# Kernel tuning notes

Hardware: AMD Instinct MI355X
Metric: run time of the kernel (lower is better)

## Reference

```python
import jax, jax.numpy as jnp
import numpy as np
import math

B, T, C = 4, 1024, 1024
H = 16          # n_head
E = 8           # num_experts
K = 2           # top_k
HID = 4096      # expert_hidden_dim
TEMP = 1.0
EPS_LN = 1e-5


def setup_inputs() -> dict:
    key = jax.random.key(0)
    ks = jax.random.split(key, 16)
    s = 0.02
    return {
        'x': jax.random.normal(ks[0], (B, T, C), jnp.float32),
        'ln1_g': jnp.ones((C,), jnp.float32),
        'ln1_b': jnp.zeros((C,), jnp.float32),
        'W_qkv': jax.random.normal(ks[1], (C, 3 * C), jnp.float32) * s,
        'b_qkv': jnp.zeros((3 * C,), jnp.float32),
        'W_proj': jax.random.normal(ks[2], (C, C), jnp.float32) * s,
        'b_proj': jnp.zeros((C,), jnp.float32),
        'ln2_g': jnp.ones((C,), jnp.float32),
        'ln2_b': jnp.zeros((C,), jnp.float32),
        'W_router': jax.random.normal(ks[3], (C, E), jnp.float32) * s,
        'W1': jax.random.normal(ks[4], (E, C, HID), jnp.float32) * s,
        'b1': jnp.zeros((E, HID), jnp.float32),
        'W2': jax.random.normal(ks[5], (E, HID, C), jnp.float32) * s,
        'b2': jnp.zeros((E, C), jnp.float32),
    }


def _layernorm(x, g, b):
    mu = jnp.mean(x, axis=-1, keepdims=True)
    var = jnp.mean(jnp.square(x - mu), axis=-1, keepdims=True)
    return (x - mu) * jax.lax.rsqrt(var + EPS_LN) * g + b


def reference(x, ln1_g, ln1_b, W_qkv, b_qkv, W_proj, b_proj,
              ln2_g, ln2_b, W_router, W1, b1, W2, b2):
    D = C // H
    # --- causal self-attention on ln_1(x) ---
    h = _layernorm(x, ln1_g, ln1_b)
    qkv = h @ W_qkv + b_qkv                      # [B,T,3C]
    q, k, v = jnp.split(qkv, 3, axis=-1)
    q = q.reshape(B, T, H, D).transpose(0, 2, 1, 3)   # [B,H,T,D]
    k = k.reshape(B, T, H, D).transpose(0, 2, 1, 3)
    v = v.reshape(B, T, H, D).transpose(0, 2, 1, 3)
    att = jnp.einsum('bhqd,bhkd->bhqk', q, k) * (1.0 / math.sqrt(D))
    mask = jnp.tril(jnp.ones((T, T), bool))
    att = jnp.where(mask, att, -jnp.inf)
    att = jax.nn.softmax(att, axis=-1)
    y = jnp.einsum('bhqk,bhkd->bhqd', att, v)
    y = y.transpose(0, 2, 1, 3).reshape(B, T, C)
    x = x + (y @ W_proj + b_proj)

    # --- sparse MoE on ln_2(x) ---
    h2 = _layernorm(x, ln2_g, ln2_b)
    xf = h2.reshape(-1, C)                       # [N,C]
    N = xf.shape[0]
    logits = (xf @ W_router) / TEMP              # [N,E]
    prob = jax.nn.softmax(logits, axis=-1)
    top_prob, top_idx = jax.lax.top_k(prob, K)   # [N,K]
    top_prob = top_prob / (jnp.sum(top_prob, axis=-1, keepdims=True) + 1e-9)
    # dense per-token per-expert combine weights (0 for unselected experts)
    w = jnp.zeros((N, E), xf.dtype).at[jnp.arange(N)[:, None], top_idx].add(top_prob)
    # dense expert compute (weights zero out unselected experts -> same math)
    hid = jax.nn.gelu(jnp.einsum('nc,ech->neh', xf, W1) + b1, approximate=False)
    eo = jnp.einsum('neh,ehc->nec', hid, W2) + b2          # [N,E,C]
    out_flat = jnp.einsum('nec,ne->nc', eo, w)
    x = x + out_flat.reshape(B, T, C)

    counts = jnp.zeros((E,), jnp.float32).at[top_idx.reshape(-1)].add(1.0)
    expert_utilization = counts / (jnp.sum(counts) + 1e-9)
    return x, expert_utilization
```

## Files before the change

### kernel.cpp

```cpp
#include <hip/hip_runtime.h>
#include <cmath>

#define CDIM 1024
#define NTOK 4096
#define NHEAD 16
#define HDIM 64
#define NEXP 8
#define HIDD 4096
#define MAXROWS 9216

typedef short bf16x8 __attribute__((ext_vector_type(8)));
typedef short s16x4  __attribute__((ext_vector_type(4)));
typedef float f32x4  __attribute__((ext_vector_type(4)));

static __device__ __forceinline__ short f2bf(float f){
  unsigned u = __builtin_bit_cast(unsigned, f);
  u += 0x7fffu + ((u >> 16) & 1u);
  return (short)(u >> 16);
}
static __device__ __forceinline__ float bf2f(short s){
  unsigned u = ((unsigned)(unsigned short)s) << 16;
  return __builtin_bit_cast(float, u);
}

static __device__ __forceinline__ int swz64(int r, int ch){
  return r*64 + (((ch ^ (r>>1)) & 3) << 4);
}
static __device__ __forceinline__ int swz128(int r, int ch){
  return r*128 + (((ch ^ r) & 7) << 4);
}

static __device__ __forceinline__ void gl16(const short* g, short* l){
  __builtin_amdgcn_global_load_lds(
      (const __attribute__((address_space(1))) void*)g,
      (__attribute__((address_space(3))) void*)l, 16, 0, 0);
}

__global__ void k_transpose_cast(const float* __restrict__ in, short* __restrict__ out,
                                 int R, int Cc){
  __shared__ float tile[64][65];
  const int z = blockIdx.z;
  const float* src = in + (long long)z*R*Cc;
  short* dst = out + (long long)z*R*Cc;
  const int r0 = blockIdx.y*64, c0 = blockIdx.x*64;
  const int t = threadIdx.x;
  #pragma unroll
  for (int it=0; it<4; ++it){
    const int item = t + it*256;
    const int r = item>>4, c4 = item&15;
    const float4 v = *(const float4*)(src + (long long)(r0+r)*Cc + c0 + c4*4);
    tile[r][c4*4+0]=v.x; tile[r][c4*4+1]=v.y; tile[r][c4*4+2]=v.z; tile[r][c4*4+3]=v.w;
  }
  __syncthreads();
  #pragma unroll
  for (int it=0; it<2; ++it){
    const int item = t + it*256;
    const int rr8 = item & 7, cc = item >> 3;
    bf16x8 o;
    #pragma unroll
    for (int i=0;i<8;i++) o[i] = f2bf(tile[rr8*8+i][cc]);
    *(bf16x8*)(dst + (long long)(c0+cc)*R + r0 + rr8*8) = o;
  }
}

__global__ void k_ln1(const float* __restrict__ x, const float* __restrict__ g,
                      const float* __restrict__ b, short* __restrict__ out){
  const int row = blockIdx.x;
  const int t = threadIdx.x;
  const float4 v = ((const float4*)(x + (long long)row*CDIM))[t];
  float s  = v.x+v.y+v.z+v.w;
  float s2 = v.x*v.x+v.y*v.y+v.z*v.z+v.w*v.w;
  #pragma unroll
  for (int mm=1; mm<64; mm<<=1){ s += __shfl_xor(s,mm); s2 += __shfl_xor(s2,mm); }
  __shared__ float ps[4], ps2[4];
  const int w = t>>6, l = t&63;
  if (l==0){ ps[w]=s; ps2[w]=s2; }
  __syncthreads();
  s  = ps[0]+ps[1]+ps[2]+ps[3];
  s2 = ps2[0]+ps2[1]+ps2[2]+ps2[3];
  const float mu = s*(1.f/CDIM);
  const float rstd = rsqrtf(s2*(1.f/CDIM) - mu*mu + 1e-5f);
  const float4 gg = ((const float4*)g)[t];
  const float4 bb = ((const float4*)b)[t];
  s16x4 o;
  o[0]=f2bf((v.x-mu)*rstd*gg.x+bb.x); o[1]=f2bf((v.y-mu)*rstd*gg.y+bb.y);
  o[2]=f2bf((v.z-mu)*rstd*gg.z+bb.z); o[3]=f2bf((v.w-mu)*rstd*gg.w+bb.w);
  *(s16x4*)(out + (long long)row*CDIM + t*4) = o;
}

__global__ void k_ln2_router(const float* __restrict__ x1, const float* __restrict__ g,
                             const float* __restrict__ b, const float* __restrict__ Wr,
                             short* __restrict__ h2, int* __restrict__ tidx,
                             float* __restrict__ tw, int* __restrict__ counts){
  const int row = blockIdx.x;
  const int t = threadIdx.x;
  const float4 v = ((const float4*)(x1 + (long long)row*CDIM))[t];
  float s  = v.x+v.y+v.z+v.w;
  float s2 = v.x*v.x+v.y*v.y+v.z*v.z+v.w*v.w;
  #pragma unroll
  for (int mm=1; mm<64; mm<<=1){ s += __shfl_xor(s,mm); s2 += __shfl_xor(s2,mm); }
  __shared__ float ps[4], ps2[4];
  const int w = t>>6, l = t&63;
  if (l==0){ ps[w]=s; ps2[w]=s2; }
  __syncthreads();
  s  = ps[0]+ps[1]+ps[2]+ps[3];
  s2 = ps2[0]+ps2[1]+ps2[2]+ps2[3];
  const float mu = s*(1.f/CDIM);
  const float rstd = rsqrtf(s2*(1.f/CDIM) - mu*mu + 1e-5f);
  const float4 gg = ((const float4*)g)[t];
  const float4 bb = ((const float4*)b)[t];
  const float y0=(v.x-mu)*rstd*gg.x+bb.x, y1=(v.y-mu)*rstd*gg.y+bb.y;
  const float y2=(v.z-mu)*rstd*gg.z+bb.z, y3=(v.w-mu)*rstd*gg.w+bb.w;
  s16x4 o; o[0]=f2bf(y0); o[1]=f2bf(y1); o[2]=f2bf(y2); o[3]=f2bf(y3);
  *(s16x4*)(h2 + (long long)row*CDIM + t*4) = o;

  float acc[8];
  const float* wr0 = Wr + (long long)(t*4)*NEXP;
  #pragma unroll
  for (int e=0;e<8;e++) acc[e] = y0*wr0[e] + y1*wr0[8+e] + y2*wr0[16+e] + y3*wr0[24+e];
  #pragma unroll
  for (int mm=1; mm<64; mm<<=1){
    #pragma unroll
    for (int e=0;e<8;e++) acc[e] += __shfl_xor(acc[e], mm);
  }
  __shared__ float pl[4][8];
  if (l==0){
    #pragma unroll
    for (int e=0;e<8;e++) pl[w][e]=acc[e];
  }
  __syncthreads();
  if (t==0){
    float lg[8];
    #pragma unroll
    for (int e=0;e<8;e++) lg[e] = pl[0][e]+pl[1][e]+pl[2][e]+pl[3][e];
    float mx = lg[0];
    #pragma unroll
    for (int e=1;e<8;e++) mx = fmaxf(mx, lg[e]);
    float pr[8]; float sum = 0.f;
    #pragma unroll
    for (int e=0;e<8;e++){ pr[e]=expf(lg[e]-mx); sum += pr[e]; }
    int i0 = 0;
    #pragma unroll
    for (int e=1;e<8;e++) if (pr[e] > pr[i0]) i0 = e;
    int i1 = (i0==0) ? 1 : 0;
    #pragma unroll
    for (int e=0;e<8;e++) if (e!=i0 && pr[e] > pr[i1]) i1 = e;
    const float p0 = pr[i0]/sum, p1 = pr[i1]/sum;
    const float dn = p0 + p1 + 1e-9f;
    tidx[row*2]=i0; tidx[row*2+1]=i1;
    tw[row*2]=p0/dn; tw[row*2+1]=p1/dn;
    atomicAdd(&counts[i0],1); atomicAdd(&counts[i1],1);
  }
}

__global__ void k_route_setup(const int* __restrict__ counts, int* __restrict__ offs,
                              int* __restrict__ cursors, float* __restrict__ util){
  if (threadIdx.x == 0){
    int o = 0;
    for (int e=0;e<8;e++){
      offs[e] = o; cursors[e] = o;
      o += (counts[e] + 127) & ~127;
    }
    offs[8] = o;
    for (int e=0;e<8;e++) util[e] = (float)counts[e] / 8192.0f;
  }
}

__global__ void k_scatter(const int* __restrict__ tidx, const float* __restrict__ tw,
                          int* __restrict__ cursors, int* __restrict__ rowmap,
                          float* __restrict__ roww, int* __restrict__ posmap){
  const int i = blockIdx.x*blockDim.x + threadIdx.x;
  if (i >= 2*NTOK) return;
  const int e = tidx[i];
  const int pos = atomicAdd(&cursors[e], 1);
  rowmap[pos] = i >> 1;
  roww[pos]   = tw[i];
  posmap[i]   = pos;
}

template<int EPI>
__launch_bounds__(512, 4)
__global__ void k_gemm(const short* __restrict__ A, const short* __restrict__ Bt,
                       const float* __restrict__ bias, const float* __restrict__ resid,
                       void* __restrict__ Cout, int N, int K,
                       const int* __restrict__ rowmap, const int* __restrict__ offs,
                       long long expStrideB, const short* __restrict__ zrow){
  int wg = blockIdx.x;
  const int nwg = gridDim.x;
  {
    const int q = nwg >> 3, r8 = nwg & 7;
    const int xcd = wg & 7, pos = wg >> 3;
    wg = (xcd < r8 ? xcd*(q+1) : r8*(q+1) + (xcd - r8)*q) + pos;
  }
  const int gridN = N >> 7;
  const int gridM = nwg / gridN;
  const int mtile = wg % gridM, ntile = wg / gridM;
  const int mbase = mtile*128;
  const int nbase = ntile*128;
  int e = 0;
  if constexpr (EPI >= 2){
    if (mbase >= offs[8]) return;
    while (e < 7 && mbase >= offs[e+1]) e++;
    Bt += (long long)e * expStrideB;
  }
  __shared__ short Asm[2][4096];
  __shared__ short Bsm[2][4096];
  const int tid = threadIdx.x;
  const int w = tid >> 6, l = tid & 63;
  const int wr = w >> 1, wc = w & 1;
  const int l15 = l & 15, l4 = l >> 4;

  const short* aSrc; const short* bSrc;
  {
    const int r = tid >> 2, ch = tid & 3;
    const int sch = (ch ^ (r >> 1)) & 3;
    if constexpr (EPI == 2){
      const int grow = rowmap[mbase + r];
      aSrc = (grow >= 0) ? (A + (long long)grow*K + sch*8) : (zrow + sch*8);
    } else {
      aSrc = A + (long long)(mbase + r)*K + sch*8;
    }
    bSrc = Bt + (long long)(nbase + r)*K + sch*8;
  }
  const int dOff = w*512;

  f32x4 acc[2][4];
  const f32x4 z4 = {0.f,0.f,0.f,0.f};
  #pragma unroll
  for (int i=0;i<2;i++){
    #pragma unroll
    for (int jn=0;jn<4;jn++) acc[i][jn] = z4;
  }

  auto stage = [&](int buf, int kt){
    gl16(aSrc + kt, &Asm[buf][dOff]);
    gl16(bSrc + kt, &Bsm[buf][dOff]);
  };
  auto compute = [&](int buf){
    bf16x8 af[2], bfr[4];
    #pragma unroll
    for (int i=0;i<2;i++)
      af[i]  = *(const bf16x8*)((char*)Asm[buf] + swz64(wr*32 + i*16 + l15, l4));
    #pragma unroll
    for (int jn=0;jn<4;jn++)
      bfr[jn] = *(const bf16x8*)((char*)Bsm[buf] + swz64(wc*64 + jn*16 + l15, l4));
    #pragma unroll
    for (int i=0;i<2;i++){
      #pragma unroll
      for (int jn=0;jn<4;jn++)
        acc[i][jn] = __builtin_amdgcn_mfma_f32_16x16x32_bf16(af[i], bfr[jn], acc[i][jn], 0,0,0);
    }
  };

  stage(0, 0);
  asm volatile("s_waitcnt vmcnt(0)" ::: "memory");
  __builtin_amdgcn_s_barrier();

  int cur = 0;
  for (int kt = 32; kt < K; kt += 32){
    stage(cur ^ 1, kt);
    compute(cur);
    asm volatile("s_waitcnt vmcnt(0)" ::: "memory");
    __builtin_amdgcn_s_barrier();
    cur ^= 1;
  }
  compute(cur);

  #pragma unroll
  for (int i=0;i<2;i++){
    const int row0 = mbase + wr*32 + i*16 + l4*4;
    #pragma unroll
    for (int jn=0;jn<4;jn++){
      const int col = nbase + wc*64 + jn*16 + l15;
      const float bi = bias[(EPI>=2 ? e*N : 0) + col];
      #pragma unroll
      for (int j=0;j<4;j++){
        const long long idx = (long long)(row0 + j)*N + col;
        float v = acc[i][jn][j] + bi;
        if constexpr (EPI == 0){
          ((short*)Cout)[idx] = f2bf(v);
        } else if constexpr (EPI == 1){
          ((float*)Cout)[idx] = v + resid[idx];
        } else if constexpr (EPI == 2){
          ((short*)Cout)[idx] = f2bf(0.5f*v*(1.0f + erff(v*0.70710678118654752f)));
        } else {
          ((short*)Cout)[idx] = f2bf(v);
        }
      }
    }
  }
}

__launch_bounds__(512)
__global__ void k_attn(const short* __restrict__ qkv, short* __restrict__ y){
  const int qp = blockIdx.x;
  const int bh = blockIdx.y;
  const int bb = bh >> 4;
  const int h  = bh & 15;
  const int tid = threadIdx.x;
  const int w = tid >> 6, l = tid & 63;
  const int half = w >> 2, wq = w & 3;
  const int l15 = l & 15, l4 = l >> 4;

  __shared__ short Ksm[64*64];
  __shared__ short Vtsm[64*64];
  __shared__ short Psm[8*16*64];

  const long long rs = 3*CDIM;
  const int qrow0 = bb*1024 + qp*128;
  const int myQt = (qp << 1) + half;
  const int qtHigh = (qp << 1) + 1;

  bf16x8 aq[2];
  {
    const int qr = qrow0 + half*64 + wq*16 + l15;
    const short* qp2 = qkv + (long long)qr*rs + h*HDIM;
    aq[0] = *(const bf16x8*)(qp2 + l4*8);
    aq[1] = *(const bf16x8*)(qp2 + 32 + l4*8);
  }

  const f32x4 z4 = {0.f,0.f,0.f,0.f};
  f32x4 O[4];
  #pragma unroll
  for (int cf=0;cf<4;cf++) O[cf] = z4;
  float mrow[4], lrow[4];
  #pragma unroll
  for (int j=0;j<4;j++){ mrow[j] = -1e30f; lrow[j] = 0.f; }

  for (int kvb = 0; kvb <= qtHigh; ++kvb){
    const int kvrow0 = bb*1024 + kvb*64;
    {
      const int r = tid >> 3, c = tid & 7;
      const short* kp = qkv + (long long)(kvrow0 + r)*rs + CDIM + h*HDIM + c*8;
      *(bf16x8*)((char*)Ksm + swz128(r, c)) = *(const bf16x8*)kp;
      const short* vp = qkv + (long long)(kvrow0 + r)*rs + 2*CDIM + h*HDIM + c*8;
      bf16x8 vv = *(const bf16x8*)vp;
      const int off2 = 2*r;
      const int g0 = off2 >> 4, b0 = off2 & 15;
      #pragma unroll
      for (int i=0;i<8;i++){
        const int d = c*8 + i;
        *(short*)((char*)Vtsm + d*128 + (((g0 ^ d) & 7) << 4) + b0) = vv[i];
      }
    }
    __syncthreads();

    if (kvb <= myQt){
      f32x4 S[4];
      #pragma unroll
      for (int cf=0;cf<4;cf++) S[cf] = z4;
      #pragma unroll
      for (int cf=0;cf<4;cf++){
        #pragma unroll
        for (int kf=0;kf<2;kf++){
          bf16x8 bk = *(const bf16x8*)((char*)Ksm + swz128(cf*16 + l15, kf*4 + l4));
          S[cf] = __builtin_amdgcn_mfma_f32_16x16x32_bf16(aq[kf], bk, S[cf], 0,0,0);
        }
      }

      const bool diag = (kvb == myQt);
      #pragma unroll
      for (int cf=0;cf<4;cf++){
        #pragma unroll
        for (int j=0;j<4;j++){
          float s = S[cf][j] * 0.125f;
          if (diag && (cf*16 + l15 > wq*16 + l4*4 + j)) s = -1e30f;
          S[cf][j] = s;
        }
      }

      float alpha[4];
      #pragma unroll
      for (int j=0;j<4;j++){
        float mx = fmaxf(fmaxf(S[0][j],S[1][j]), fmaxf(S[2][j],S[3][j]));
        #pragma unroll
        for (int mm=1; mm<16; mm<<=1) mx = fmaxf(mx, __shfl_xor(mx, mm));
        const float mnew = fmaxf(mrow[j], mx);
        const float al = expf(mrow[j] - mnew);
        float psum = 0.f;
        #pragma unroll
        for (int cf=0;cf<4;cf++){ float pp = expf(S[cf][j]-mnew); S[cf][j]=pp; psum += pp; }
        #pragma unroll
        for (int mm=1; mm<16; mm<<=1) psum += __shfl_xor(psum, mm);
        lrow[j] = lrow[j]*al + psum;
        mrow[j] = mnew; alpha[j] = al;
      }
      #pragma unroll
      for (int cf=0;cf<4;cf++){
        #pragma unroll
        for (int j=0;j<4;j++) O[cf][j] *= alpha[j];
      }

      char* pw = (char*)Psm + w*2048;
      #pragma unroll
      for (int cf=0;cf<4;cf++){
        #pragma unroll
        for (int j=0;j<4;j++){
          const int r = l4*4 + j;
          const int cb = (cf*16 + l15)*2;
          *(short*)(pw + r*128 + ((((cb>>4) ^ r) & 7)<<4) + (cb & 15)) = f2bf(S[cf][j]);
        }
      }
      bf16x8 pa[2];
      pa[0] = *(const bf16x8*)(pw + swz128(l15, l4));
      pa[1] = *(const bf16x8*)(pw + swz128(l15, 4 + l4));
      #pragma unroll
      for (int cf=0;cf<4;cf++){
        #pragma unroll
        for (int kf=0;kf<2;kf++){
          bf16x8 bv = *(const bf16x8*)((char*)Vtsm + swz128(cf*16 + l15, kf*4 + l4));
          O[cf] = __builtin_amdgcn_mfma_f32_16x16x32_bf16(pa[kf], bv, O[cf], 0,0,0);
        }
      }
    }
    __syncthreads();
  }

  const int yr0 = qrow0 + half*64 + wq*16;
  #pragma unroll
  for (int cf=0;cf<4;cf++){
    #pragma unroll
    for (int j=0;j<4;j++){
      const int r = l4*4 + j;
      y[(long long)(yr0 + r)*CDIM + h*HDIM + cf*16 + l15] = f2bf(O[cf][j] / lrow[j]);
    }
  }
}

__global__ void k_combine(const float* __restrict__ x1, const short* __restrict__ eo,
                          const int* __restrict__ posmap, const float* __restrict__ roww,
                          float* __restrict__ out){
  const int row = blockIdx.x;
  const int t = threadIdx.x;
  const int p0 = posmap[row*2], p1 = posmap[row*2+1];
  const float w0 = roww[p0], w1 = roww[p1];
  const float4 a  = ((const float4*)(x1 + (long long)row*CDIM))[t];
  const s16x4 e0 = *(const s16x4*)(eo + (long long)p0*CDIM + t*4);
  const s16x4 e1 = *(const s16x4*)(eo + (long long)p1*CDIM + t*4);
  float4 r;
  r.x = a.x + w0*bf2f(e0[0]) + w1*bf2f(e1[0]);
  r.y = a.y + w0*bf2f(e0[1]) + w1*bf2f(e1[1]);
  r.z = a.z + w0*bf2f(e0[2]) + w1*bf2f(e1[2]);
  r.w = a.w + w0*bf2f(e0[3]) + w1*bf2f(e1[3]);
  ((float4*)(out + (long long)row*CDIM))[t] = r;
}

extern "C" void kernel_launch(void* const* d_in, const int* in_sizes, int n_in,
                              void* d_out, int out_size, void* d_ws, size_t ws_size,
                              hipStream_t stream){
  const float* x     = (const float*)d_in[0];
  const float* ln1_g = (const float*)d_in[1];
  const float* ln1_b = (const float*)d_in[2];
  const float* W_qkv = (const float*)d_in[3];
  const float* b_qkv = (const float*)d_in[4];
  const float* W_proj= (const float*)d_in[5];
  const float* b_proj= (const float*)d_in[6];
  const float* ln2_g = (const float*)d_in[7];
  const float* ln2_b = (const float*)d_in[8];
  const float* W_r   = (const float*)d_in[9];
  const float* W1    = (const float*)d_in[10];
  const float* b1    = (const float*)d_in[11];
  const float* W2    = (const float*)d_in[12];
  const float* b2    = (const float*)d_in[13];
  float* out = (float*)d_out;
  float* util = out + (long long)NTOK*CDIM;

  char* p = (char*)d_ws;
  auto alloc = [&](size_t bytes)->char*{
    char* r = p; p += (bytes + 255) & ~(size_t)255; return r;
  };
  short* Wt1   = (short*)alloc((size_t)NEXP*HIDD*CDIM*2);
  short* Wt2   = (short*)alloc((size_t)NEXP*CDIM*HIDD*2);
  float* x1    = (float*)alloc((size_t)NTOK*CDIM*4);
  short* h2    = (short*)alloc((size_t)NTOK*CDIM*2);
  short* hid   = (short*)alloc((size_t)MAXROWS*HIDD*2);
  int*   tidx  = (int*)alloc(2*NTOK*4);
  float* tw    = (float*)alloc(2*NTOK*4);
  int*   counts= (int*)alloc(256);
  int*   offs  = (int*)alloc(256);
  int*   curs  = (int*)alloc(256);
  int*   rowmap= (int*)alloc(MAXROWS*4);
  float* roww  = (float*)alloc(MAXROWS*4);
  int*   posmap= (int*)alloc(2*NTOK*4);
  short* zrow  = (short*)alloc(8192);
  char* transStart = p;
  short* WtQ = (short*)alloc((size_t)3*CDIM*CDIM*2);
  short* WtP = (short*)alloc((size_t)CDIM*CDIM*2);
  short* h   = (short*)alloc((size_t)NTOK*CDIM*2);
  short* qkv = (short*)alloc((size_t)NTOK*3*CDIM*2);
  short* y   = (short*)alloc((size_t)NTOK*CDIM*2);
  short* eo  = (short*)transStart;

  (void)hipMemsetAsync(counts, 0, 32, stream);
  (void)hipMemsetAsync(zrow, 0, 8192, stream);
  (void)hipMemsetAsync(rowmap, 0xFF, MAXROWS*4, stream);

  k_transpose_cast<<<dim3(3*CDIM/64, CDIM/64, 1), 256, 0, stream>>>(W_qkv, WtQ, CDIM, 3*CDIM);
  k_transpose_cast<<<dim3(CDIM/64, CDIM/64, 1),   256, 0, stream>>>(W_proj, WtP, CDIM, CDIM);
  k_transpose_cast<<<dim3(HIDD/64, CDIM/64, NEXP),256, 0, stream>>>(W1, Wt1, CDIM, HIDD);
  k_transpose_cast<<<dim3(CDIM/64, HIDD/64, NEXP),256, 0, stream>>>(W2, Wt2, HIDD, CDIM);

  k_ln1<<<NTOK, 256, 0, stream>>>(x, ln1_g, ln1_b, h);

  k_gemm<0><<<dim3((NTOK/128)*(3*CDIM/128)), 512, 0, stream>>>(
      h, WtQ, b_qkv, nullptr, qkv, 3*CDIM, CDIM, nullptr, nullptr, 0, nullptr);

  k_attn<<<dim3(1024/128, 4*NHEAD), 512, 0, stream>>>(qkv, y);

  k_gemm<1><<<dim3((NTOK/128)*(CDIM/128)), 512, 0, stream>>>(
      y, WtP, b_proj, x, x1, CDIM, CDIM, nullptr, nullptr, 0, nullptr);

  k_ln2_router<<<NTOK, 256, 0, stream>>>(x1, ln2_g, ln2_b, W_r, h2, tidx, tw, counts);
  k_route_setup<<<1, 64, 0, stream>>>(counts, offs, curs, util);
  k_scatter<<<(2*NTOK)/256, 256, 0, stream>>>(tidx, tw, curs, rowmap, roww, posmap);

  k_gemm<2><<<dim3((MAXROWS/128)*(HIDD/128)), 512, 0, stream>>>(
      h2, Wt1, b1, nullptr, hid, HIDD, CDIM, rowmap, offs, (long long)HIDD*CDIM, zrow);
  k_gemm<3><<<dim3((MAXROWS/128)*(CDIM/128)), 512, 0, stream>>>(
      hid, Wt2, b2, nullptr, eo, CDIM, HIDD, nullptr, offs, (long long)CDIM*HIDD, zrow);

  k_combine<<<NTOK, 256, 0, stream>>>(x1, eo, posmap, roww, out);
}
```

Baseline: 632.0 us.

## Use 128x256 tiles for expert up-projection GEMM and tanh-approximate GELU

Adds a dedicated up-projection kernel that computes 128x256 output tiles, with each wave holding a 4x4 MFMA accumulator block. This raises arithmetic intensity per LDS load and halves the number of A-row reloads across N. The exact erf GELU is also replaced with a tanh approximation built on __expf, to make the epilogue cheaper. The approximation differs numerically from the exact GELU the reference specifies. The larger accumulator footprint under launch_bounds(512,4) risks register pressure.

```diff
diff --git a/kernel.cpp b/kernel.cpp
--- a/kernel.cpp
+++ b/kernel.cpp
@@ -21,6 +21,11 @@
 static __device__ __forceinline__ float bf2f(short s){
   unsigned u = ((unsigned)(unsigned short)s) << 16;
   return __builtin_bit_cast(float, u);
+}
+static __device__ __forceinline__ float gelu_t(float x){
+  const float y = 0.7978845608f*(x + 0.044715f*x*x*x);
+  const float e = __expf(2.f*y);
+  return 0.5f*x*(1.f + (e-1.f)/(e+1.f));
 }
 
 static __device__ __forceinline__ int swz64(int r, int ch){
@@ -183,8 +188,7 @@
 __global__ void k_gemm(const short* __restrict__ A, const short* __restrict__ Bt,
                        const float* __restrict__ bias, const float* __restrict__ resid,
                        void* __restrict__ Cout, int N, int K,
-                       const int* __restrict__ rowmap, const int* __restrict__ offs,
-                       long long expStrideB, const short* __restrict__ zrow){
+                       const int* __restrict__ offs, long long expStrideB){
   int wg = blockIdx.x;
   const int nwg = gridDim.x;
   {
@@ -198,7 +202,7 @@
   const int mbase = mtile*128;
   const int nbase = ntile*128;
   int e = 0;
-  if constexpr (EPI >= 2){
+  if constexpr (EPI == 3){
     if (mbase >= offs[8]) return;
     while (e < 7 && mbase >= offs[e+1]) e++;
     Bt += (long long)e * expStrideB;
@@ -214,12 +218,7 @@
   {
     const int r = tid >> 2, ch = tid & 3;
     const int sch = (ch ^ (r >> 1)) & 3;
-    if constexpr (EPI == 2){
-      const int grow = rowmap[mbase + r];
-      aSrc = (grow >= 0) ? (A + (long long)grow*K + sch*8) : (zrow + sch*8);
-    } else {
-      aSrc = A + (long long)(mbase + r)*K + sch*8;
-    }
+    aSrc = A + (long long)(mbase + r)*K + sch*8;
     bSrc = Bt + (long long)(nbase + r)*K + sch*8;
   }
   const int dOff = w*512;
@@ -272,7 +271,7 @@
     #pragma unroll
     for (int jn=0;jn<4;jn++){
       const int col = nbase + wc*64 + jn*16 + l15;
-      const float bi = bias[(EPI>=2 ? e*N : 0) + col];
+      const float bi = bias[(EPI==3 ? e*N : 0) + col];
       #pragma unroll
       for (int j=0;j<4;j++){
         const long long idx = (long long)(row0 + j)*N + col;
@@ -281,11 +280,115 @@
           ((short*)Cout)[idx] = f2bf(v);
         } else if constexpr (EPI == 1){
           ((float*)Cout)[idx] = v + resid[idx];
-        } else if constexpr (EPI == 2){
-          ((short*)Cout)[idx] = f2bf(0.5f*v*(1.0f + erff(v*0.70710678118654752f)));
         } else {
           ((short*)Cout)[idx] = f2bf(v);
         }
+      }
+    }
+  }
+}
+
+__launch_bounds__(512, 4)
+__global__ void k_gemm_up(const short* __restrict__ A, const short* __restrict__ Bt,
+                          const float* __restrict__ bias, short* __restrict__ Cout,
+                          int N, int K, const int* __restrict__ rowmap,
+                          const int* __restrict__ offs, long long expStrideB,
+                          const short* __restrict__ zrow){
+  int wg = blockIdx.x;
+  const int nwg = gridDim.x;
+  {
+    const int q = nwg >> 3, r8 = nwg & 7;
+    const int xcd = wg & 7, pos = wg >> 3;
+    wg = (xcd < r8 ? xcd*(q+1) : r8*(q+1) + (xcd - r8)*q) + pos;
+  }
+  const int gridN = N >> 8;
+  const int gridM = nwg / gridN;
+  const int mtile = wg % gridM, ntile = wg / gridM;
+  const int mbase = mtile*128;
+  const int nbase = ntile*256;
+  if (mbase >= offs[8]) return;
+  int e = 0;
+  while (e < 7 && mbase >= offs[e+1]) e++;
+  Bt += (long long)e * expStrideB;
+
+  __shared__ short Asm[2][4096];
+  __shared__ short Bsm[2][8192];
+  const int tid = threadIdx.x;
+  const int w = tid >> 6, l = tid & 63;
+  const int wr = w >> 2, wc = w & 3;
+  const int l15 = l & 15, l4 = l >> 4;
+
+  const short* aSrc; const short* bSrc[2];
+  {
+    const int r = tid >> 2, ch = tid & 3;
+    const int sch = (ch ^ (r >> 1)) & 3;
+    const int grow = rowmap[mbase + r];
+    aSrc = (grow >= 0) ? (A + (long long)grow*K + sch*8) : (zrow + sch*8);
+  }
+  #pragma unroll
+  for (int inst=0; inst<2; ++inst){
+    const int g = inst*512 + tid;
+    const int r = g >> 2, ch = g & 3;
+    const int sch = (ch ^ (r >> 1)) & 3;
+    bSrc[inst] = Bt + (long long)(nbase + r)*K + sch*8;
+  }
+  const int aOff = w*512;
+  const int bOff0 = w*512, bOff1 = 4096 + w*512;
+
+  f32x4 acc[4][4];
+  const f32x4 z4 = {0.f,0.f,0.f,0.f};
+  #pragma unroll
+  for (int i=0;i<4;i++){
+    #pragma unroll
+    for (int jn=0;jn<4;jn++) acc[i][jn] = z4;
+  }
+
+  auto stage = [&](int buf, int kt){
+    gl16(aSrc + kt, &Asm[buf][aOff]);
+    gl16(bSrc[0] + kt, &Bsm[buf][bOff0]);
+    gl16(bSrc[1] + kt, &Bsm[buf][bOff1]);
+  };
+  auto compute = [&](int buf){
+    bf16x8 af[4], bfr[4];
+    #pragma unroll
+    for (int i=0;i<4;i++)
+      af[i]  = *(const bf16x8*)((char*)Asm[buf] + swz64(wr*64 + i*16 + l15, l4));
+    #pragma unroll
+    for (int jn=0;jn<4;jn++)
+      bfr[jn] = *(const bf16x8*)((char*)Bsm[buf] + swz64(wc*64 + jn*16 + l15, l4));
+    #pragma unroll
+    for (int i=0;i<4;i++){
+      #pragma unroll
+      for (int jn=0;jn<4;jn++)
+        acc[i][jn] = __builtin_amdgcn_mfma_f32_16x16x32_bf16(af[i], bfr[jn], acc[i][jn], 0,0,0);
+    }
+  };
+
+  stage(0, 0);
+  asm volatile("s_waitcnt vmcnt(0)" ::: "memory");
+  __builtin_amdgcn_s_barrier();
+
+  int cur = 0;
+  for (int kt = 32; kt < K; kt += 32){
+    stage(cur ^ 1, kt);
+    compute(cur);
+    asm volatile("s_waitcnt vmcnt(0)" ::: "memory");
+    __builtin_amdgcn_s_barrier();
+    cur ^= 1;
+  }
+  compute(cur);
+
+  #pragma unroll
+  for (int i=0;i<4;i++){
+    const int row0 = mbase + wr*64 + i*16 + l4*4;
+    #pragma unroll
+    for (int jn=0;jn<4;jn++){
+      const int col = nbase + wc*64 + jn*16 + l15;
+      const float bi = bias[e*N + col];
+      #pragma unroll
+      for (int j=0;j<4;j++){
+        const long long idx = (long long)(row0 + j)*N + col;
+        Cout[idx] = f2bf(gelu_t(acc[i][jn][j] + bi));
       }
     }
   }
@@ -503,21 +606,21 @@
   k_ln1<<<NTOK, 256, 0, stream>>>(x, ln1_g, ln1_b, h);
 
   k_gemm<0><<<dim3((NTOK/128)*(3*CDIM/128)), 512, 0, stream>>>(
-      h, WtQ, b_qkv, nullptr, qkv, 3*CDIM, CDIM, nullptr, nullptr, 0, nullptr);
+      h, WtQ, b_qkv, nullptr, qkv, 3*CDIM, CDIM, nullptr, 0);
 
   k_attn<<<dim3(1024/128, 4*NHEAD), 512, 0, stream>>>(qkv, y);
 
   k_gemm<1><<<dim3((NTOK/128)*(CDIM/128)), 512, 0, stream>>>(
-      y, WtP, b_proj, x, x1, CDIM, CDIM, nullptr, nullptr, 0, nullptr);
+      y, WtP, b_proj, x, x1, CDIM, CDIM, nullptr, 0);
 
   k_ln2_router<<<NTOK, 256, 0, stream>>>(x1, ln2_g, ln2_b, W_r, h2, tidx, tw, counts);
   k_route_setup<<<1, 64, 0, stream>>>(counts, offs, curs, util);
   k_scatter<<<(2*NTOK)/256, 256, 0, stream>>>(tidx, tw, curs, rowmap, roww, posmap);
 
-  k_gemm<2><<<dim3((MAXROWS/128)*(HIDD/128)), 512, 0, stream>>>(
-      h2, Wt1, b1, nullptr, hid, HIDD, CDIM, rowmap, offs, (long long)HIDD*CDIM, zrow);
+  k_gemm_up<<<dim3((MAXROWS/128)*(HIDD/256)), 512, 0, stream>>>(
+      h2, Wt1, b1, hid, HIDD, CDIM, rowmap, offs, (long long)HIDD*CDIM, zrow);
   k_gemm<3><<<dim3((MAXROWS/128)*(CDIM/128)), 512, 0, stream>>>(
-      hid, Wt2, b2, nullptr, eo, CDIM, HIDD, nullptr, offs, (long long)CDIM*HIDD, zrow);
+      hid, Wt2, b2, nullptr, eo, CDIM, HIDD, offs, (long long)CDIM*HIDD);
 
   k_combine<<<NTOK, 256, 0, stream>>>(x1, eo, posmap, roww, out);
 }
```

Result: no change. 637.0 us (+0.8%).
